# Optimization experiments

Hardware: AMD Instinct MI355X
Metric: run time of the kernel (lower is better)

Reference implementation:

```python
import jax, jax.numpy as jnp
import numpy as np

G = 16          # horizontal stripes
K = 4           # latents per stripe
TEMP = 0.125
TOPK_RATIO = 0.125
GATE_THR = 0.05
EPS = 1e-6
KSZ = 3


def setup_inputs() -> dict:
    key = jax.random.key(0)
    k1, k2 = jax.random.split(key)
    x = jax.random.normal(k1, (64, 256, 64, 44), dtype=jnp.float32)
    latent_basis = jax.random.normal(k2, (G, K, 256), dtype=jnp.float32)
    return {"x": x, "latent_basis": latent_basis}


def _avg_pool3(x):
    # x: [n, g, c, sh, w]; 3x3 avg pool, stride 1, pad 1, count_include_pad=True
    s = jax.lax.reduce_window(x, 0.0, jax.lax.add,
                              (1, 1, 1, KSZ, KSZ), (1, 1, 1, 1, 1),
                              [(0, 0), (0, 0), (0, 0), (1, 1), (1, 1)])
    return s / float(KSZ * KSZ)


def _l2norm(v, axis=-1):
    return v / jnp.maximum(jnp.linalg.norm(v, axis=axis, keepdims=True), 1e-12)


def reference(x, latent_basis):
    n, c, h, w = x.shape
    sh = h // G
    p = sh * w
    # split into horizontal stripes: [n, g, c, sh, w]
    xr = x.reshape(n, c, G, sh, w).transpose(0, 2, 1, 3, 4)
    support_feat = _avg_pool3(xr)
    feat_flat = xr.transpose(0, 1, 3, 4, 2).reshape(n, G, p, c)          # ngpc
    support_flat = support_feat.transpose(0, 1, 3, 4, 2).reshape(n, G, p, c)

    # active mask from detached feature energy
    e = jax.lax.stop_gradient(xr).astype(jnp.float32)
    fe = jnp.mean(e * e, axis=2)                                          # n g sh w
    fe = fe / jnp.maximum(jnp.max(fe, axis=(-2, -1), keepdims=True), EPS)
    active = (fe > GATE_THR).astype(jnp.float32)
    fallback = (fe > 0).astype(jnp.float32)
    use_fb = jnp.sum(active, axis=(-2, -1), keepdims=True) <= 0
    active = jnp.where(use_fb, fallback, active).reshape(n, G, p)

    # cosine-similarity routing
    sfn = _l2norm(support_flat)
    lbn = _l2norm(latent_basis)                                           # g k c
    logits = jnp.einsum('ngpc,gkc->ngpk', sfn, lbn) / TEMP
    route_prob = jax.nn.softmax(logits, axis=-1)
    support = route_prob * active[..., None]                              # n g p k
    pool_w = support / jnp.maximum(jnp.sum(support, axis=2, keepdims=True), EPS)
    tokens = jnp.einsum('ngpk,ngpc->ngkc', pool_w, feat_flat)
    tokens = tokens.transpose(0, 3, 1, 2).reshape(n, c, G * K)            # n c (g k)

    # top-k presence
    kk = max(1, min(p, int(p * TOPK_RATIO)))
    topv, _ = jax.lax.top_k(support.transpose(0, 1, 3, 2), kk)            # n g k kk
    presence = jnp.mean(topv, axis=-1).reshape(n, G * K)
    presence = presence / jnp.maximum(jnp.sum(presence, axis=1, keepdims=True), EPS)

    # scatter per-stripe maps back into full-resolution zero tensors
    eye = jnp.eye(G, dtype=support.dtype)
    loc_s = support.reshape(n, G, sh, w, K).transpose(0, 1, 4, 2, 3)      # n g k sh w
    loc_p = pool_w.reshape(n, G, sh, w, K).transpose(0, 1, 4, 2, 3)
    smap = jnp.einsum('ngksw,gG->ngkGsw', loc_s, eye).reshape(n, G * K, h, w)
    pmap = jnp.einsum('ngksw,gG->ngkGsw', loc_p, eye).reshape(n, G * K, h, w)
    support_flat_global = smap.transpose(0, 2, 3, 1).reshape(n, h * w, G * K)
    pool_weights_flat_global = pmap.transpose(0, 2, 3, 1).reshape(n, h * w, G * K)

    return (tokens.astype(x.dtype), presence.astype(x.dtype),
            support_flat_global.astype(x.dtype), pool_weights_flat_global.astype(x.dtype))
```

## Files before the change

kernel.cpp:

```cpp
#include <hip/hip_runtime.h>
#include <math.h>

#define GG   16
#define KK   4
#define NN   64
#define CC   256
#define SHH  4
#define WW   44
#define PP   176
#define HWSZ 2816
#define CHW  720896
#define TOPKK 22

template<int CTRL, int RMASK>
__device__ __forceinline__ float dpp0(float v) {
    return __int_as_float(__builtin_amdgcn_update_dpp(
        0, __float_as_int(v), CTRL, RMASK, 0xF, true));
}
__device__ __forceinline__ float nbrL(float v) { return dpp0<0x138, 0xF>(v); }
__device__ __forceinline__ float nbrR(float v) { return dpp0<0x130, 0xF>(v); }

__device__ __forceinline__ float wave_sum63(float v) {
    v += dpp0<0x111, 0xF>(v);
    v += dpp0<0x112, 0xF>(v);
    v += dpp0<0x114, 0xF>(v);
    v += dpp0<0x118, 0xF>(v);
    v += dpp0<0x142, 0xA>(v);
    v += dpp0<0x143, 0xC>(v);
    return v;
}
__device__ __forceinline__ float bcast63(float v) {
    return __int_as_float(__builtin_amdgcn_readlane(__float_as_int(v), 63));
}
__device__ __forceinline__ float wave_sum_all(float v) { return bcast63(wave_sum63(v)); }

__device__ __forceinline__ float wave_max_nn(float v) {
    v = fmaxf(v, dpp0<0x111, 0xF>(v));
    v = fmaxf(v, dpp0<0x112, 0xF>(v));
    v = fmaxf(v, dpp0<0x114, 0xF>(v));
    v = fmaxf(v, dpp0<0x118, 0xF>(v));
    v = fmaxf(v, dpp0<0x142, 0xA>(v));
    v = fmaxf(v, dpp0<0x143, 0xC>(v));
    return bcast63(v);
}

__global__ __launch_bounds__(512, 8) void routing_kernel(
    const float* __restrict__ x, const float* __restrict__ lb_raw,
    float* __restrict__ pres_ws,
    float4* __restrict__ outS, float4* __restrict__ outP,
    float* __restrict__ tok_out) {
    const int g = blockIdx.x;
    const int n = blockIdx.y;
    const int tid = threadIdx.x;
    const int w = __builtin_amdgcn_readfirstlane(tid >> 6);
    const int lane = tid & 63;
    const bool al = lane < WW;

    __shared__ float4 pd[8][PP];
    __shared__ float2 pnf[8][PP];
    __shared__ float4 lbn_lds[CC];
    __shared__ float redA[4], redB[4], zred[4][4];
    float4* sup4 = pd[2];
    float4* pw4  = pd[4];
    float4* pwT  = pd[6];

    if (w < 4) {
        const float* row = lb_raw + ((size_t)g * KK + w) * CC;
        float v0 = row[lane], v1 = row[lane + 64], v2 = row[lane + 128], v3 = row[lane + 192];
        float ss = v0 * v0 + v1 * v1 + v2 * v2 + v3 * v3;
        float tot = wave_sum_all(ss);
        float sc = (1.0f / 9.0f) / fmaxf(sqrtf(tot), 1e-12f);
        float* dst = (float*)lbn_lds;
        dst[lane * 4 + w]         = v0 * sc;
        dst[(lane + 64) * 4 + w]  = v1 * sc;
        dst[(lane + 128) * 4 + w] = v2 * sc;
        dst[(lane + 192) * 4 + w] = v3 * sc;
    }
    __syncthreads();

    const float* xb = x + (size_t)n * CHW + g * PP;
    const int c0 = w * 32;

    float4 dk[4];
    float nr[4] = {0, 0, 0, 0}, fe[4] = {0, 0, 0, 0};
    #pragma unroll
    for (int s = 0; s < 4; ++s) dk[s] = make_float4(0, 0, 0, 0);

    const float* xp = xb + (size_t)c0 * HWSZ + lane;
    float c0r = 0, c1r = 0, c2r = 0, c3r = 0;
    float n0r = 0, n1r = 0, n2r = 0, n3r = 0;
    float m0r = 0, m1r = 0, m2r = 0, m3r = 0;
    if (al) {
        c0r = xp[0]; c1r = xp[44]; c2r = xp[88]; c3r = xp[132];
        n0r = xp[HWSZ]; n1r = xp[HWSZ + 44]; n2r = xp[HWSZ + 88]; n3r = xp[HWSZ + 132];
        m0r = xp[2 * HWSZ]; m1r = xp[2 * HWSZ + 44]; m2r = xp[2 * HWSZ + 88]; m3r = xp[2 * HWSZ + 132];
    }
    xp += 3 * HWSZ;
    #pragma unroll 1
    for (int i = 0; i < 32; ++i) {
        float f0 = 0, f1 = 0, f2 = 0, f3 = 0;
        if (i < 29 && al) { f0 = xp[0]; f1 = xp[44]; f2 = xp[88]; f3 = xp[132]; }
        xp += HWSZ;
        float4 lbv = lbn_lds[c0 + i];
        fe[0] += c0r * c0r; fe[1] += c1r * c1r; fe[2] += c2r * c2r; fe[3] += c3r * c3r;
        float h0 = c0r + nbrL(c0r) + nbrR(c0r);
        float h1 = c1r + nbrL(c1r) + nbrR(c1r);
        float h2 = c2r + nbrL(c2r) + nbrR(c2r);
        float h3 = c3r + nbrL(c3r) + nbrR(c3r);
        float p0 = h0 + h1;
        float p1 = p0 + h2;
        float t23 = h2 + h3;
        float p2 = h1 + t23;
        float p3 = t23;
        nr[0] += p0 * p0; nr[1] += p1 * p1; nr[2] += p2 * p2; nr[3] += p3 * p3;
        dk[0].x += p0 * lbv.x; dk[0].y += p0 * lbv.y; dk[0].z += p0 * lbv.z; dk[0].w += p0 * lbv.w;
        dk[1].x += p1 * lbv.x; dk[1].y += p1 * lbv.y; dk[1].z += p1 * lbv.z; dk[1].w += p1 * lbv.w;
        dk[2].x += p2 * lbv.x; dk[2].y += p2 * lbv.y; dk[2].z += p2 * lbv.z; dk[2].w += p2 * lbv.w;
        dk[3].x += p3 * lbv.x; dk[3].y += p3 * lbv.y; dk[3].z += p3 * lbv.z; dk[3].w += p3 * lbv.w;
        c0r = n0r; c1r = n1r; c2r = n2r; c3r = n3r;
        n0r = m0r; n1r = m1r; n2r = m2r; n3r = m3r;
        m0r = f0; m1r = f1; m2r = f2; m3r = f3;
    }
    if (al) {
        #pragma unroll
        for (int s = 0; s < 4; ++s) {
            pd[w][s * 44 + lane]  = dk[s];
            pnf[w][s * 44 + lane] = make_float2(nr[s], fe[s]);
        }
    }
    __syncthreads();

    if (tid < PP) {
        float4 a = pd[0][tid];
        #pragma unroll
        for (int ww = 1; ww < 8; ++ww) {
            float4 b = pd[ww][tid];
            a.x += b.x; a.y += b.y; a.z += b.z; a.w += b.w;
        }
        pd[0][tid] = a;
    } else if (tid >= 256 && tid < 256 + PP) {
        const int p = tid - 256;
        float2 a = pnf[0][p];
        #pragma unroll
        for (int ww = 1; ww < 8; ++ww) {
            float2 b = pnf[ww][p];
            a.x += b.x; a.y += b.y;
        }
        pnf[0][p] = a;
    }
    __syncthreads();

    const int s4 = w & 3;
    const int pix = s4 * 44 + (al ? lane : 0);
    float4 dv = pd[0][pix];
    float2 nf = pnf[0][pix];
    float nrm = nf.x;
    float fev = nf.y * (1.0f / 256.0f);

    float fmw = wave_max_nn(al ? fev : 0.0f);
    if (w < 4 && lane == 0) redA[s4] = fmw;
    __syncthreads();
    float femax = fmaxf(fmaxf(redA[0], redA[1]), fmaxf(redA[2], redA[3]));
    float den = fmaxf(femax, 1e-6f);
    bool pa = al && ((fev / den) > 0.05f);
    unsigned long long bl = __ballot((int)pa);
    if (w < 4 && lane == 0) redB[s4] = (float)__popcll(bl);
    __syncthreads();
    float cnt = redB[0] + redB[1] + redB[2] + redB[3];
    float actv = pa ? 1.0f : 0.0f;
    if (cnt <= 0.0f) actv = (al && (fev > 0.0f)) ? 1.0f : 0.0f;

    float inv = 72.0f / fmaxf(sqrtf(nrm), 9e-12f);
    float L0 = dv.x * inv, L1 = dv.y * inv, L2 = dv.z * inv, L3 = dv.w * inv;
    float mx = fmaxf(fmaxf(L0, L1), fmaxf(L2, L3));
    float e0 = expf(L0 - mx), e1 = expf(L1 - mx), e2 = expf(L2 - mx), e3 = expf(L3 - mx);
    float esum = e0 + e1 + e2 + e3;
    float sc = actv / esum;
    float s0 = e0 * sc, s1 = e1 * sc, s2 = e2 * sc, s3 = e3 * sc;

    float z0 = wave_sum63(s0), z1 = wave_sum63(s1), z2 = wave_sum63(s2), z3 = wave_sum63(s3);
    if (w < 4 && lane == 63) { zred[s4][0] = z0; zred[s4][1] = z1; zred[s4][2] = z2; zred[s4][3] = z3; }
    __syncthreads();
    float Z0 = zred[0][0] + zred[1][0] + zred[2][0] + zred[3][0];
    float Z1 = zred[0][1] + zred[1][1] + zred[2][1] + zred[3][1];
    float Z2 = zred[0][2] + zred[1][2] + zred[2][2] + zred[3][2];
    float Z3 = zred[0][3] + zred[1][3] + zred[2][3] + zred[3][3];
    float q0 = s0 / fmaxf(Z0, 1e-6f);
    float q1 = s1 / fmaxf(Z1, 1e-6f);
    float q2 = s2 / fmaxf(Z2, 1e-6f);
    float q3 = s3 / fmaxf(Z3, 1e-6f);

    if (w < 4 && al) {
        float4 qv = make_float4(q0, q1, q2, q3);
        sup4[pix] = make_float4(s0, s1, s2, s3);
        pw4[pix]  = qv;
        pwT[(pix & 3) * 44 + (pix >> 2)] = qv;
    }
    __syncthreads();

    if (w < 4) {
        const float* supf = (const float*)sup4;
        const int k = w;
        float v0 = supf[lane * 4 + k];
        float v1 = supf[(lane + 64) * 4 + k];
        float v2 = (lane < PP - 128) ? supf[(lane + 128) * 4 + k] : -1e30f;
        float tks = 0.0f;
        for (int it = 0; it < TOPKK; ++it) {
            float lm = fmaxf(v0, fmaxf(v1, v2));
            float M = wave_max_nn(lm);
            tks += M;
            unsigned long long mk = __ballot((int)(lm == M));
            int src = __ffsll(mk) - 1;
            if (lane == src) {
                if (v0 == M)      v0 = -1e30f;
                else if (v1 == M) v1 = -1e30f;
                else              v2 = -1e30f;
            }
        }
        if (lane == 0) pres_ws[(size_t)n * 64 + g * KK + k] = tks * (1.0f / (float)TOPKK);
    } else {
        const size_t obase = ((size_t)n * HWSZ + (size_t)g * PP) * 16;
        const float4 z = make_float4(0, 0, 0, 0);
        const int t0i = tid - 256;
        #pragma unroll 1
        for (int m = 0; m < 11; ++m) {
            const int j = t0i + m * 256;
            const int px = j >> 4, q = j & 15;
            const bool hit = (q == g);
            outS[obase + j] = hit ? sup4[px] : z;
            outP[obase + j] = hit ? pw4[px]  : z;
        }
    }

    {
        const bool a4 = lane < 44;
        float4 pwa = make_float4(0, 0, 0, 0), pwb = pwa, pwc = pwa, pwd = pwa;
        if (a4) {
            pwa = pwT[lane];
            pwb = pwT[44 + lane];
            pwc = pwT[88 + lane];
            pwd = pwT[132 + lane];
        }
        const float4* xq4 = (const float4*)(xb + (size_t)c0 * HWSZ) + lane;
        float4 tA = make_float4(0, 0, 0, 0), tB = tA, tC = tA;
        if (a4) { tA = xq4[0]; tB = xq4[704]; tC = xq4[1408]; }
        xq4 += 3 * 704;
        float* tokg = tok_out + ((size_t)n * CC + c0) * 64 + g * KK;

        #pragma unroll 1
        for (int i = 0; i < 32; ++i) {
            float4 tF = make_float4(0, 0, 0, 0);
            if (i < 29 && a4) tF = xq4[0];
            xq4 += 704;
            float t0 = tA.x * pwa.x + tA.y * pwb.x + tA.z * pwc.x + tA.w * pwd.x;
            float t1 = tA.x * pwa.y + tA.y * pwb.y + tA.z * pwc.y + tA.w * pwd.y;
            float t2 = tA.x * pwa.z + tA.y * pwb.z + tA.z * pwc.z + tA.w * pwd.z;
            float t3 = tA.x * pwa.w + tA.y * pwb.w + tA.z * pwc.w + tA.w * pwd.w;
            t0 = wave_sum63(t0); t1 = wave_sum63(t1); t2 = wave_sum63(t2); t3 = wave_sum63(t3);
            if (lane == 63) {
                *(float4*)(tokg + (size_t)i * 64) = make_float4(t0, t1, t2, t3);
            }
            tA = tB; tB = tC; tC = tF;
        }
    }
}

__global__ __launch_bounds__(64) void presence_kernel(
    const float* __restrict__ pres_ws, float* __restrict__ outp) {
    const int n = blockIdx.x;
    const int lane = threadIdx.x;
    float v = pres_ws[(size_t)n * 64 + lane];
    float tot = wave_sum_all(v);
    outp[(size_t)n * 64 + lane] = v / fmaxf(tot, 1e-6f);
}

extern "C" void kernel_launch(void* const* d_in, const int* in_sizes, int n_in,
                              void* d_out, int out_size, void* d_ws, size_t ws_size,
                              hipStream_t stream) {
    const float* x = (const float*)d_in[0];
    const float* lb = (const float*)d_in[1];
    float* ws = (float*)d_ws;
    float* pres_ws = ws;

    float* out = (float*)d_out;
    float* tok  = out;
    float* pres = out + 1048576;
    float* outS = out + 1052672;
    float* outP = outS + 11534336;

    routing_kernel<<<dim3(GG, NN), 512, 0, stream>>>(
        x, lb, pres_ws, (float4*)outS, (float4*)outP, tok);
    presence_kernel<<<NN, 64, 0, stream>>>(pres_ws, pres);
}
```

Baseline: 335.4 us.

## Stage x in LDS as bf16 for reuse in the token pass

During the routing pass, waves 0–4 write their channels of x into a dynamic-shared-memory buffer as bf16. The token-pooling pass then reads those 160 channels from LDS instead of reloading them from global memory; waves 5–7 still reload their channels from global. The cross-wave partial reduction is reworked to use 4 LDS slots with a two-step accumulate, which shrinks that scratch area. In exchange, the block now needs about 77 KB of LDS, launch bounds drop to 2 blocks per CU, and tokens are computed from bf16-rounded x, which loses precision.

After: 329.4 us. No clear change (-1.8%).

```diff
diff --git a/kernel.cpp b/kernel.cpp
--- a/kernel.cpp
+++ b/kernel.cpp
@@ -12,6 +12,9 @@
 #define CHW  720896
 #define TOPKK 22
 
+#define NSTAGE_CH 160
+#define SMEM_BYTES 77408
+
 template<int CTRL, int RMASK>
 __device__ __forceinline__ float dpp0(float v) {
     return __int_as_float(__builtin_amdgcn_update_dpp(
@@ -44,7 +47,13 @@
     return bcast63(v);
 }
 
-__global__ __launch_bounds__(512, 8) void routing_kernel(
+__device__ __forceinline__ unsigned short bf16rne(float f) {
+    unsigned u = __float_as_uint(f);
+    u += 0x7FFFu + ((u >> 16) & 1u);
+    return (unsigned short)(u >> 16);
+}
+
+__global__ __launch_bounds__(512, 2) void routing_kernel(
     const float* __restrict__ x, const float* __restrict__ lb_raw,
     float* __restrict__ pres_ws,
     float4* __restrict__ outS, float4* __restrict__ outP,
@@ -56,13 +65,17 @@
     const int lane = tid & 63;
     const bool al = lane < WW;
 
-    __shared__ float4 pd[8][PP];
-    __shared__ float2 pnf[8][PP];
-    __shared__ float4 lbn_lds[CC];
-    __shared__ float redA[4], redB[4], zred[4][4];
-    float4* sup4 = pd[2];
-    float4* pw4  = pd[4];
-    float4* pwT  = pd[6];
+    extern __shared__ char smem_raw[];
+    float4* pd      = (float4*)smem_raw;
+    float2* pnf     = (float2*)(smem_raw + 11264);
+    float4* lbn_lds = (float4*)(smem_raw + 16896);
+    float*  redA    = (float*)(smem_raw + 20992);
+    float*  redB    = redA + 4;
+    float*  zred    = redB + 4;
+    unsigned short* xst = (unsigned short*)(smem_raw + 21088);
+    float4* sup4 = pd + 1 * PP;
+    float4* pw4  = pd + 2 * PP;
+    float4* pwT  = pd + 3 * PP;
 
     if (w < 4) {
         const float* row = lb_raw + ((size_t)g * KK + w) * CC;
@@ -80,6 +93,7 @@
 
     const float* xb = x + (size_t)n * CHW + g * PP;
     const int c0 = w * 32;
+    const bool stager = (w < 5);
 
     float4 dk[4];
     float nr[4] = {0, 0, 0, 0}, fe[4] = {0, 0, 0, 0};
@@ -102,6 +116,13 @@
         if (i < 29 && al) { f0 = xp[0]; f1 = xp[44]; f2 = xp[88]; f3 = xp[132]; }
         xp += HWSZ;
         float4 lbv = lbn_lds[c0 + i];
+        if (stager && al) {
+            unsigned short* xrow = xst + (size_t)(c0 + i) * PP + lane;
+            xrow[0]   = bf16rne(c0r);
+            xrow[44]  = bf16rne(c1r);
+            xrow[88]  = bf16rne(c2r);
+            xrow[132] = bf16rne(c3r);
+        }
         fe[0] += c0r * c0r; fe[1] += c1r * c1r; fe[2] += c2r * c2r; fe[3] += c3r * c3r;
         float h0 = c0r + nbrL(c0r) + nbrR(c0r);
         float h1 = c1r + nbrL(c1r) + nbrR(c1r);
@@ -121,39 +142,53 @@
         n0r = m0r; n1r = m1r; n2r = m2r; n3r = m3r;
         m0r = f0; m1r = f1; m2r = f2; m3r = f3;
     }
-    if (al) {
+    if (w < 4 && al) {
         #pragma unroll
         for (int s = 0; s < 4; ++s) {
-            pd[w][s * 44 + lane]  = dk[s];
-            pnf[w][s * 44 + lane] = make_float2(nr[s], fe[s]);
+            pd[w * PP + s * 44 + lane]  = dk[s];
+            pnf[w * PP + s * 44 + lane] = make_float2(nr[s], fe[s]);
+        }
+    }
+    __syncthreads();
+    if (w >= 4 && al) {
+        const int wb = (w - 4) * PP;
+        #pragma unroll
+        for (int s = 0; s < 4; ++s) {
+            const int idx = wb + s * 44 + lane;
+            float4 a = pd[idx];
+            a.x += dk[s].x; a.y += dk[s].y; a.z += dk[s].z; a.w += dk[s].w;
+            pd[idx] = a;
+            float2 b = pnf[idx];
+            b.x += nr[s]; b.y += fe[s];
+            pnf[idx] = b;
         }
     }
     __syncthreads();
 
     if (tid < PP) {
-        float4 a = pd[0][tid];
+        float4 a = pd[tid];
         #pragma unroll
-        for (int ww = 1; ww < 8; ++ww) {
-            float4 b = pd[ww][tid];
+        for (int ww = 1; ww < 4; ++ww) {
+            float4 b = pd[ww * PP + tid];
             a.x += b.x; a.y += b.y; a.z += b.z; a.w += b.w;
         }
-        pd[0][tid] = a;
+        pd[tid] = a;
     } else if (tid >= 256 && tid < 256 + PP) {
         const int p = tid - 256;
-        float2 a = pnf[0][p];
+        float2 a = pnf[p];
         #pragma unroll
-        for (int ww = 1; ww < 8; ++ww) {
-            float2 b = pnf[ww][p];
+        for (int ww = 1; ww < 4; ++ww) {
+            float2 b = pnf[ww * PP + p];
             a.x += b.x; a.y += b.y;
         }
-        pnf[0][p] = a;
+        pnf[p] = a;
     }
     __syncthreads();
 
     const int s4 = w & 3;
     const int pix = s4 * 44 + (al ? lane : 0);
-    float4 dv = pd[0][pix];
-    float2 nf = pnf[0][pix];
+    float4 dv = pd[pix];
+    float2 nf = pnf[pix];
     float nrm = nf.x;
     float fev = nf.y * (1.0f / 256.0f);
 
@@ -179,12 +214,15 @@
     float s0 = e0 * sc, s1 = e1 * sc, s2 = e2 * sc, s3 = e3 * sc;
 
     float z0 = wave_sum63(s0), z1 = wave_sum63(s1), z2 = wave_sum63(s2), z3 = wave_sum63(s3);
-    if (w < 4 && lane == 63) { zred[s4][0] = z0; zred[s4][1] = z1; zred[s4][2] = z2; zred[s4][3] = z3; }
-    __syncthreads();
-    float Z0 = zred[0][0] + zred[1][0] + zred[2][0] + zred[3][0];
-    float Z1 = zred[0][1] + zred[1][1] + zred[2][1] + zred[3][1];
-    float Z2 = zred[0][2] + zred[1][2] + zred[2][2] + zred[3][2];
-    float Z3 = zred[0][3] + zred[1][3] + zred[2][3] + zred[3][3];
+    if (w < 4 && lane == 63) {
+        zred[s4 * 4 + 0] = z0; zred[s4 * 4 + 1] = z1;
+        zred[s4 * 4 + 2] = z2; zred[s4 * 4 + 3] = z3;
+    }
+    __syncthreads();
+    float Z0 = zred[0] + zred[4] + zred[8]  + zred[12];
+    float Z1 = zred[1] + zred[5] + zred[9]  + zred[13];
+    float Z2 = zred[2] + zred[6] + zred[10] + zred[14];
+    float Z3 = zred[3] + zred[7] + zred[11] + zred[15];
     float q0 = s0 / fmaxf(Z0, 1e-6f);
     float q1 = s1 / fmaxf(Z1, 1e-6f);
     float q2 = s2 / fmaxf(Z2, 1e-6f);
@@ -233,34 +271,56 @@
     }
 
     {
-        const bool a4 = lane < 44;
         float4 pwa = make_float4(0, 0, 0, 0), pwb = pwa, pwc = pwa, pwd = pwa;
-        if (a4) {
+        if (al) {
             pwa = pwT[lane];
             pwb = pwT[44 + lane];
             pwc = pwT[88 + lane];
             pwd = pwT[132 + lane];
         }
-        const float4* xq4 = (const float4*)(xb + (size_t)c0 * HWSZ) + lane;
-        float4 tA = make_float4(0, 0, 0, 0), tB = tA, tC = tA;
-        if (a4) { tA = xq4[0]; tB = xq4[704]; tC = xq4[1408]; }
-        xq4 += 3 * 704;
         float* tokg = tok_out + ((size_t)n * CC + c0) * 64 + g * KK;
 
-        #pragma unroll 1
-        for (int i = 0; i < 32; ++i) {
-            float4 tF = make_float4(0, 0, 0, 0);
-            if (i < 29 && a4) tF = xq4[0];
-            xq4 += 704;
-            float t0 = tA.x * pwa.x + tA.y * pwb.x + tA.z * pwc.x + tA.w * pwd.x;
-            float t1 = tA.x * pwa.y + tA.y * pwb.y + tA.z * pwc.y + tA.w * pwd.y;
-            float t2 = tA.x * pwa.z + tA.y * pwb.z + tA.z * pwc.z + tA.w * pwd.z;
-            float t3 = tA.x * pwa.w + tA.y * pwb.w + tA.z * pwc.w + tA.w * pwd.w;
-            t0 = wave_sum63(t0); t1 = wave_sum63(t1); t2 = wave_sum63(t2); t3 = wave_sum63(t3);
-            if (lane == 63) {
-                *(float4*)(tokg + (size_t)i * 64) = make_float4(t0, t1, t2, t3);
+        if (stager) {
+            const unsigned short* xr = xst + (size_t)c0 * PP + 4 * (al ? lane : 0);
+            #pragma unroll 1
+            for (int i = 0; i < 32; ++i) {
+                float b0 = 0, b1 = 0, b2 = 0, b3 = 0;
+                if (al) {
+                    ushort4 v = *(const ushort4*)(xr + (size_t)i * PP);
+                    b0 = __uint_as_float((unsigned)v.x << 16);
+                    b1 = __uint_as_float((unsigned)v.y << 16);
+                    b2 = __uint_as_float((unsigned)v.z << 16);
+                    b3 = __uint_as_float((unsigned)v.w << 16);
+                }
+                float t0 = b0 * pwa.x + b1 * pwb.x + b2 * pwc.x + b3 * pwd.x;
+                float t1 = b0 * pwa.y + b1 * pwb.y + b2 * pwc.y + b3 * pwd.y;
+                float t2 = b0 * pwa.z + b1 * pwb.z + b2 * pwc.z + b3 * pwd.z;
+                float t3 = b0 * pwa.w + b1 * pwb.w + b2 * pwc.w + b3 * pwd.w;
+                t0 = wave_sum63(t0); t1 = wave_sum63(t1); t2 = wave_sum63(t2); t3 = wave_sum63(t3);
+                if (lane == 63) {
+                    *(float4*)(tokg + (size_t)i * 64) = make_float4(t0, t1, t2, t3);
+                }
             }
-            tA = tB; tB = tC; tC = tF;
+        } else {
+            const float4* xq4 = (const float4*)(xb + (size_t)c0 * HWSZ) + lane;
+            float4 tA = make_float4(0, 0, 0, 0), tB = tA, tC = tA;
+            if (al) { tA = xq4[0]; tB = xq4[704]; tC = xq4[1408]; }
+            xq4 += 3 * 704;
+            #pragma unroll 1
+            for (int i = 0; i < 32; ++i) {
+                float4 tF = make_float4(0, 0, 0, 0);
+                if (i < 29 && al) tF = xq4[0];
+                xq4 += 704;
+                float t0 = tA.x * pwa.x + tA.y * pwb.x + tA.z * pwc.x + tA.w * pwd.x;
+                float t1 = tA.x * pwa.y + tA.y * pwb.y + tA.z * pwc.y + tA.w * pwd.y;
+                float t2 = tA.x * pwa.z + tA.y * pwb.z + tA.z * pwc.z + tA.w * pwd.z;
+                float t3 = tA.x * pwa.w + tA.y * pwb.w + tA.z * pwc.w + tA.w * pwd.w;
+                t0 = wave_sum63(t0); t1 = wave_sum63(t1); t2 = wave_sum63(t2); t3 = wave_sum63(t3);
+                if (lane == 63) {
+                    *(float4*)(tokg + (size_t)i * 64) = make_float4(t0, t1, t2, t3);
+                }
+                tA = tB; tB = tC; tC = tF;
+            }
         }
     }
 }
@@ -288,7 +348,15 @@
     float* outS = out + 1052672;
     float* outP = outS + 11534336;
 
-    routing_kernel<<<dim3(GG, NN), 512, 0, stream>>>(
+    static bool attr_set = false;
+    if (!attr_set) {
+        hipFuncSetAttribute((const void*)routing_kernel,
+                            hipFuncAttributeMaxDynamicSharedMemorySize,
+                            SMEM_BYTES);
+        attr_set = true;
+    }
+
+    routing_kernel<<<dim3(GG, NN), 512, SMEM_BYTES, stream>>>(
         x, lb, pres_ws, (float4*)outS, (float4*)outP, tok);
     presence_kernel<<<NN, 64, 0, stream>>>(pres_ws, pres);
 }
```
